# Kernel tuning notes

Hardware: AMD Instinct MI355X
Metric: run time of the kernel (lower is better)

The kernel has to match this reference:

```python
import jax, jax.numpy as jnp
import numpy as np

B, D, E, K = 8192, 4096, 64, 2

def setup_inputs() -> dict:
    key = jax.random.key(0)
    k1, k2 = jax.random.split(key)
    x = jax.random.normal(k1, (B, D), dtype=jnp.float32)
    gate_w = jax.random.normal(k2, (E, D), dtype=jnp.float32) * (1.0 / np.sqrt(D))
    temperature = jnp.ones((), dtype=jnp.float32)
    return {"x": x, "gate_w": gate_w, "temperature": temperature}

def reference(x, gate_w, temperature):
    # logits = (x @ W^T) / temperature  -> [B, E]
    logits = jnp.einsum('bd,ed->be', x, gate_w) / temperature
    top_logits, top_idx = jax.lax.top_k(logits, K)          # [B, K]
    routing_weights = jax.nn.softmax(top_logits, axis=-1)    # [B, K]
    rows = jnp.arange(x.shape[0])[:, None]                   # [B, 1]
    routing_matrix = jnp.zeros((x.shape[0], E), dtype=x.dtype).at[rows, top_idx].set(routing_weights)
    return routing_matrix, top_idx
```

## Files before the change

### kernel.cpp

```cpp
#include <hip/hip_runtime.h>
#include <stdint.h>
#include <stddef.h>


typedef __attribute__((ext_vector_type(8))) short short8;
typedef __attribute__((ext_vector_type(4))) float f32x4;

static constexpr int kB = 8192;
static constexpr int kD = 4096;
static constexpr int kE = 64;
static constexpr int kSteps = kD / 32;
static constexpr int kKS = 8;
static constexpr int kSPS = kSteps / kKS;
static constexpr int kRG = 64;
static constexpr int kRPB = kB / kRG;

__device__ __forceinline__ uint32_t bf16_rne(float v) {
    uint32_t u = __builtin_bit_cast(uint32_t, v);
    return (u + 0x7FFFu + ((u >> 16) & 1u)) >> 16;
}

__device__ __forceinline__ void cvt8(const f32x4& a0, const f32x4& a1,
                                     short8& ah, short8& al) {
#pragma unroll
    for (int j = 0; j < 4; ++j) {
        float xv = a0[j];
        uint32_t u  = __builtin_bit_cast(uint32_t, xv);
        uint32_t rh = (u + 0x7FFFu + ((u >> 16) & 1u)) & 0xFFFF0000u;
        ah[j] = (short)(rh >> 16);
        al[j] = (short)bf16_rne(xv - __builtin_bit_cast(float, rh));
        float yv = a1[j];
        uint32_t u2  = __builtin_bit_cast(uint32_t, yv);
        uint32_t rh2 = (u2 + 0x7FFFu + ((u2 >> 16) & 1u)) & 0xFFFF0000u;
        ah[j + 4] = (short)(rh2 >> 16);
        al[j + 4] = (short)bf16_rne(yv - __builtin_bit_cast(float, rh2));
    }
}

__global__ __launch_bounds__(256) void prep_w_kernel(
    const float* __restrict__ w, short* __restrict__ w_hi, short* __restrict__ w_lo)
{
    int tid  = blockIdx.x * 256 + threadIdx.x;
    int lane = tid & 63;
    int s    = (tid >> 6) & (kSteps - 1);
    int nt   = tid >> 13;
    int e = nt * 16 + (lane & 15);
    int k = s * 32 + (lane >> 4) * 8;
    const float* src = w + (size_t)e * kD + k;
    short8 hi, lo;
#pragma unroll
    for (int j = 0; j < 8; ++j) {
        float xv = src[j];
        uint32_t u  = __builtin_bit_cast(uint32_t, xv);
        uint32_t rh = (u + 0x7FFFu + ((u >> 16) & 1u)) & 0xFFFF0000u;
        hi[j] = (short)(rh >> 16);
        float lf = xv - __builtin_bit_cast(float, rh);
        lo[j] = (short)bf16_rne(lf);
    }
    ((short8*)w_hi)[tid] = hi;
    ((short8*)w_lo)[tid] = lo;
}

__global__ __launch_bounds__(512, 4) void gemm_partial(
    const float* __restrict__ x, const short8* __restrict__ w_hi,
    const short8* __restrict__ w_lo, float* __restrict__ part)
{
    const int lane = threadIdx.x & 63;
    const int mt   = threadIdx.x >> 6;
    const int quad = lane >> 4;
    const int mr   = lane & 15;
    const int ks   = blockIdx.x >> 6;
    const int rg   = blockIdx.x & 63;

    const int row0 = rg * kRPB + mt * 16;
    const float* xp = x + (size_t)(row0 + mr) * kD + ks * (kSPS * 32) + quad * 8;

    f32x4 acc[4];
#pragma unroll
    for (int nt = 0; nt < 4; ++nt) acc[nt] = (f32x4){0.f, 0.f, 0.f, 0.f};

    f32x4  xb[2][2];
    short8 wbh[2][4], wbl[2][4];

#pragma unroll
    for (int s = 0; s < 2; ++s) {
        const f32x4* ap = (const f32x4*)(xp + s * 32);
        xb[s][0] = ap[0];
        xb[s][1] = ap[1];
        const size_t S = (size_t)(ks * kSPS + s);
#pragma unroll
        for (int nt = 0; nt < 4; ++nt) {
            wbh[s][nt] = w_hi[(size_t)(nt * kSteps) * 64 + S * 64 + lane];
            wbl[s][nt] = w_lo[(size_t)(nt * kSteps) * 64 + S * 64 + lane];
        }
    }

#pragma unroll
    for (int s = 0; s < kSPS; ++s) {
        const int slot = s & 1;
        short8 ah, al;
        cvt8(xb[slot][0], xb[slot][1], ah, al);
#pragma unroll
        for (int nt = 0; nt < 4; ++nt) {
            acc[nt] = __builtin_amdgcn_mfma_f32_16x16x32_bf16(al, wbl[slot][nt], acc[nt], 0, 0, 0);
            acc[nt] = __builtin_amdgcn_mfma_f32_16x16x32_bf16(al, wbh[slot][nt], acc[nt], 0, 0, 0);
            acc[nt] = __builtin_amdgcn_mfma_f32_16x16x32_bf16(ah, wbl[slot][nt], acc[nt], 0, 0, 0);
            acc[nt] = __builtin_amdgcn_mfma_f32_16x16x32_bf16(ah, wbh[slot][nt], acc[nt], 0, 0, 0);
        }
        if (s + 2 < kSPS) {
            const f32x4* ap = (const f32x4*)(xp + (s + 2) * 32);
            xb[slot][0] = ap[0];
            xb[slot][1] = ap[1];
            const size_t S = (size_t)(ks * kSPS + s + 2);
#pragma unroll
            for (int nt = 0; nt < 4; ++nt) {
                wbh[slot][nt] = w_hi[(size_t)(nt * kSteps) * 64 + S * 64 + lane];
                wbl[slot][nt] = w_lo[(size_t)(nt * kSteps) * 64 + S * 64 + lane];
            }
        }
    }

    float* pp = part + ((size_t)ks * kB + row0) * kE;
#pragma unroll
    for (int nt = 0; nt < 4; ++nt)
#pragma unroll
        for (int r = 0; r < 4; ++r)
            pp[(size_t)(quad * 4 + r) * kE + nt * 16 + mr] = acc[nt][r];
}

__global__ __launch_bounds__(256) void reduce_top2(
    const float* __restrict__ part, const float* __restrict__ temp,
    float* __restrict__ out_mat, float* __restrict__ out_idx)
{
    const int lane = threadIdx.x & 63;
    const int wv   = threadIdx.x >> 6;
    const float invT = 1.0f / temp[0];

#pragma unroll
    for (int i = 0; i < 4; ++i) {
        const int row = blockIdx.x * 16 + wv * 4 + i;
        float v = 0.f;
#pragma unroll
        for (int ks = 0; ks < kKS; ++ks)
            v += part[((size_t)ks * kB + row) * kE + lane];

        float v1 = v; int i1 = lane;
#pragma unroll
        for (int m = 1; m < 64; m <<= 1) {
            float ov = __shfl_xor(v1, m, 64);
            int   oi = __shfl_xor(i1, m, 64);
            if (ov > v1 || (ov == v1 && oi < i1)) { v1 = ov; i1 = oi; }
        }
        float vm = (lane == i1) ? -3.0e38f : v;
        float v2 = vm; int i2 = lane;
#pragma unroll
        for (int m = 1; m < 64; m <<= 1) {
            float ov = __shfl_xor(v2, m, 64);
            int   oi = __shfl_xor(i2, m, 64);
            if (ov > v2 || (ov == v2 && oi < i2)) { v2 = ov; i2 = oi; }
        }

        float e  = expf((v2 - v1) * invT);
        float sm = 1.0f + e;
        out_mat[(size_t)row * kE + lane] =
            (lane == i1) ? (1.0f / sm) : ((lane == i2) ? (e / sm) : 0.0f);
        if (lane == 0)
            ((float2*)out_idx)[row] = make_float2((float)i1, (float)i2);
    }
}

extern "C" void kernel_launch(void* const* d_in, const int* in_sizes, int n_in,
                              void* d_out, int out_size, void* d_ws, size_t ws_size,
                              hipStream_t stream) {
    const float* x    = (const float*)d_in[0];
    const float* gw   = (const float*)d_in[1];
    const float* temp = (const float*)d_in[2];

    float* out_mat = (float*)d_out;
    float* out_idx = (float*)d_out + (size_t)kB * kE;

    short* w_hi = (short*)d_ws;
    short* w_lo = w_hi + (size_t)kE * kD;
    float* part = (float*)(w_lo + (size_t)kE * kD);

    prep_w_kernel<<<128, 256, 0, stream>>>(gw, w_hi, w_lo);

    gemm_partial<<<kRG * kKS, 512, 0, stream>>>(
        x, (const short8*)w_hi, (const short8*)w_lo, part);

    reduce_top2<<<512, 256, 0, stream>>>(part, temp, out_mat, out_idx);
}
```

Measured before the change: 218.9 us.

## Stage x tiles through LDS with async global_load_lds and per-wave K-split

Result: no change. 217.5 us (-0.7%).

```diff
diff --git a/kernel.cpp b/kernel.cpp
--- a/kernel.cpp
+++ b/kernel.cpp
@@ -12,8 +12,7 @@
 static constexpr int kSteps = kD / 32;
 static constexpr int kKS = 8;
 static constexpr int kSPS = kSteps / kKS;
-static constexpr int kRG = 64;
-static constexpr int kRPB = kB / kRG;
+static constexpr int kMT = kB / 16;
 
 __device__ __forceinline__ uint32_t bf16_rne(float v) {
     uint32_t u = __builtin_bit_cast(uint32_t, v);
@@ -37,6 +36,12 @@
     }
 }
 
+__device__ __forceinline__ void glds16(const float* g, float* l) {
+    __builtin_amdgcn_global_load_lds(
+        (const __attribute__((address_space(1))) unsigned int*)g,
+        (__attribute__((address_space(3))) unsigned int*)l, 16, 0, 0);
+}
+
 __global__ __launch_bounds__(256) void prep_w_kernel(
     const float* __restrict__ w, short* __restrict__ w_hi, short* __restrict__ w_lo)
 {
@@ -66,61 +71,75 @@
     const short8* __restrict__ w_lo, float* __restrict__ part)
 {
     const int lane = threadIdx.x & 63;
-    const int mt   = threadIdx.x >> 6;
+    const int wv   = threadIdx.x >> 6;
     const int quad = lane >> 4;
     const int mr   = lane & 15;
-    const int ks   = blockIdx.x >> 6;
-    const int rg   = blockIdx.x & 63;
-
-    const int row0 = rg * kRPB + mt * 16;
-    const float* xp = x + (size_t)(row0 + mr) * kD + ks * (kSPS * 32) + quad * 8;
+    const int row0 = blockIdx.x * 16;
+
+    __shared__ __align__(16) float smem[kKS * 4 * 512];
+    float* ring = &smem[wv * 4 * 512];
+
+    const int gr  = lane >> 3;
+    const int gc  = (lane & 7) ^ gr;
+    const float* gbase0 = x + (size_t)(row0 + gr) * kD + wv * (kSPS * 32) + gc * 4;
+    const float* gbase1 = gbase0 + (size_t)8 * kD;
+
+    const int p0 = ((2 * quad) ^ (mr & 7)) * 4 + mr * 32;
+    const int p1 = ((2 * quad + 1) ^ (mr & 7)) * 4 + mr * 32;
 
     f32x4 acc[4];
 #pragma unroll
     for (int nt = 0; nt < 4; ++nt) acc[nt] = (f32x4){0.f, 0.f, 0.f, 0.f};
 
-    f32x4  xb[2][2];
     short8 wbh[2][4], wbl[2][4];
 
 #pragma unroll
     for (int s = 0; s < 2; ++s) {
-        const f32x4* ap = (const f32x4*)(xp + s * 32);
-        xb[s][0] = ap[0];
-        xb[s][1] = ap[1];
-        const size_t S = (size_t)(ks * kSPS + s);
+        glds16(gbase0 + s * 32, ring + s * 512);
+        glds16(gbase1 + s * 32, ring + s * 512 + 256);
+    }
+    {
+        const size_t S = (size_t)(wv * kSPS);
 #pragma unroll
         for (int nt = 0; nt < 4; ++nt) {
-            wbh[s][nt] = w_hi[(size_t)(nt * kSteps) * 64 + S * 64 + lane];
-            wbl[s][nt] = w_lo[(size_t)(nt * kSteps) * 64 + S * 64 + lane];
+            wbh[0][nt] = w_hi[(size_t)(nt * kSteps + S) * 64 + lane];
+            wbl[0][nt] = w_lo[(size_t)(nt * kSteps + S) * 64 + lane];
         }
     }
 
 #pragma unroll
     for (int s = 0; s < kSPS; ++s) {
-        const int slot = s & 1;
+        const int slot = s & 3;
+        const int wsl  = s & 1;
+        if (s + 2 < kSPS) {
+            const int sl2 = (s + 2) & 3;
+            glds16(gbase0 + (s + 2) * 32, ring + sl2 * 512);
+            glds16(gbase1 + (s + 2) * 32, ring + sl2 * 512 + 256);
+        }
+        if (s + 1 < kSPS) {
+            const size_t S = (size_t)(wv * kSPS + s + 1);
+#pragma unroll
+            for (int nt = 0; nt < 4; ++nt) {
+                wbh[wsl ^ 1][nt] = w_hi[(size_t)(nt * kSteps + S) * 64 + lane];
+                wbl[wsl ^ 1][nt] = w_lo[(size_t)(nt * kSteps + S) * 64 + lane];
+            }
+        }
+        asm volatile("s_waitcnt vmcnt(10)" ::: "memory");
+
+        f32x4 a0 = *(const f32x4*)(ring + slot * 512 + p0);
+        f32x4 a1 = *(const f32x4*)(ring + slot * 512 + p1);
         short8 ah, al;
-        cvt8(xb[slot][0], xb[slot][1], ah, al);
+        cvt8(a0, a1, ah, al);
 #pragma unroll
         for (int nt = 0; nt < 4; ++nt) {
-            acc[nt] = __builtin_amdgcn_mfma_f32_16x16x32_bf16(al, wbl[slot][nt], acc[nt], 0, 0, 0);
-            acc[nt] = __builtin_amdgcn_mfma_f32_16x16x32_bf16(al, wbh[slot][nt], acc[nt], 0, 0, 0);
-            acc[nt] = __builtin_amdgcn_mfma_f32_16x16x32_bf16(ah, wbl[slot][nt], acc[nt], 0, 0, 0);
-            acc[nt] = __builtin_amdgcn_mfma_f32_16x16x32_bf16(ah, wbh[slot][nt], acc[nt], 0, 0, 0);
-        }
-        if (s + 2 < kSPS) {
-            const f32x4* ap = (const f32x4*)(xp + (s + 2) * 32);
-            xb[slot][0] = ap[0];
-            xb[slot][1] = ap[1];
-            const size_t S = (size_t)(ks * kSPS + s + 2);
-#pragma unroll
-            for (int nt = 0; nt < 4; ++nt) {
-                wbh[slot][nt] = w_hi[(size_t)(nt * kSteps) * 64 + S * 64 + lane];
-                wbl[slot][nt] = w_lo[(size_t)(nt * kSteps) * 64 + S * 64 + lane];
-            }
-        }
-    }
-
-    float* pp = part + ((size_t)ks * kB + row0) * kE;
+            acc[nt] = __builtin_amdgcn_mfma_f32_16x16x32_bf16(al, wbl[wsl][nt], acc[nt], 0, 0, 0);
+            acc[nt] = __builtin_amdgcn_mfma_f32_16x16x32_bf16(al, wbh[wsl][nt], acc[nt], 0, 0, 0);
+            acc[nt] = __builtin_amdgcn_mfma_f32_16x16x32_bf16(ah, wbl[wsl][nt], acc[nt], 0, 0, 0);
+            acc[nt] = __builtin_amdgcn_mfma_f32_16x16x32_bf16(ah, wbh[wsl][nt], acc[nt], 0, 0, 0);
+        }
+    }
+
+    float* pp = part + ((size_t)wv * kB + row0) * kE;
 #pragma unroll
     for (int nt = 0; nt < 4; ++nt)
 #pragma unroll
@@ -185,7 +204,7 @@
 
     prep_w_kernel<<<128, 256, 0, stream>>>(gw, w_hi, w_lo);
 
-    gemm_partial<<<kRG * kKS, 512, 0, stream>>>(
+    gemm_partial<<<kMT, 512, 0, stream>>>(
         x, (const short8*)w_hi, (const short8*)w_lo, part);
 
     reduce_top2<<<512, 256, 0, stream>>>(part, temp, out_mat, out_idx);
```
